# Kernel optimization log

Hardware: AMD Instinct MI355X
Metric: run time of the kernel (lower is better)

The kernel has to match this reference:

```python
import jax, jax.numpy as jnp
import numpy as np

B, N, D, H, NC = 4, 32, 128, 8, 27
DK = D // H
DFF = 4 * D
L = NC * N


def layer_norm(x, g, b, eps=1e-5):
    mu = jnp.mean(x, -1, keepdims=True)
    var = jnp.var(x, -1, keepdims=True)
    return (x - mu) * jax.lax.rsqrt(var + eps) * g + b


def setup_inputs() -> dict:
    ks = jax.random.split(jax.random.key(0), 16)
    s = 1.0 / np.sqrt(D)
    return {
        'x': jax.random.normal(ks[0], (B, N, D), jnp.float32),
        'mask': jax.random.randint(ks[1], (B, 1, N), 0, 2, jnp.int32),
        'coords': jax.random.normal(ks[2], (B, NC, N, 3), jnp.float32),
        'Wp': jax.random.normal(ks[3], (3, D), jnp.float32) * 0.5,
        'bp': jnp.zeros((D,), jnp.float32),
        'Wq': jax.random.normal(ks[4], (D, D), jnp.float32) * s,
        'bq': jnp.zeros((D,), jnp.float32),
        'Wk': jax.random.normal(ks[5], (D, D), jnp.float32) * s,
        'bk': jnp.zeros((D,), jnp.float32),
        'Wv': jax.random.normal(ks[6], (D, D), jnp.float32) * s,
        'bv': jnp.zeros((D,), jnp.float32),
        'Wo': jax.random.normal(ks[7], (D, D), jnp.float32) * s,
        'bo': jnp.zeros((D,), jnp.float32),
        'g1': jnp.ones((D,), jnp.float32),
        'b1': jnp.zeros((D,), jnp.float32),
        'g2': jnp.ones((D,), jnp.float32),
        'b2': jnp.zeros((D,), jnp.float32),
        'W1': jax.random.normal(ks[8], (D, DFF), jnp.float32) * s,
        'bf1': jnp.zeros((DFF,), jnp.float32),
        'W2': jax.random.normal(ks[9], (DFF, D), jnp.float32) * (1.0 / np.sqrt(DFF)),
        'bf2': jnp.zeros((D,), jnp.float32),
    }


def reference(x, mask, coords, Wp, bp, Wq, bq, Wk, bk, Wv, bv, Wo, bo,
              g1, b1, g2, b2, W1, bf1, W2, bf2):
    mask_enh = jnp.tile(mask, (1, NC, 1)).reshape(B, 1, 1, L)

    def step(i):
        # position_encoding: x broadcast over 27 images + linear of coords relative to atom i
        ci = jax.lax.dynamic_slice_in_dim(coords, i, 1, axis=2)        # [B,NC,1,3]
        ar = x[:, None] + (coords - ci) @ Wp + bp                      # [B,NC,N,D]
        a = ar.reshape(B, L, D)
        hn = layer_norm(a, g1, b1)
        q = (hn @ Wq + bq).reshape(B, L, H, DK).transpose(0, 2, 1, 3)
        k = (hn @ Wk + bk).reshape(B, L, H, DK).transpose(0, 2, 1, 3)
        v = (hn @ Wv + bv).reshape(B, L, H, DK).transpose(0, 2, 1, 3)
        scores = jnp.einsum('bhqd,bhkd->bhqk', q, k) / np.sqrt(DK)     # [B,H,L,L]
        scores = jnp.where(mask_enh == 0, -1e9, scores)
        att = jnp.einsum('bhqk,bhkd->bhqd', jax.nn.softmax(scores, -1), v)
        att = att.transpose(0, 2, 1, 3).reshape(B, L, D) @ Wo + bo
        s = a + att  # SublayerConnection (dropout identity in eval)
        # original keeps only [b, image 0, atom i] of the [B,NC,N,D] reshape; flat index = i
        return jax.lax.dynamic_slice_in_dim(s, i, 1, axis=1)[:, 0]     # [B,D]

    rows = jax.lax.map(step, jnp.arange(N))                            # [N,B,D]
    y = rows.transpose(1, 0, 2)                                        # [B,N,D]
    hn2 = layer_norm(y, g2, b2)
    return y + (jax.nn.relu(hn2 @ W1 + bf1) @ W2 + bf2)
```

## Files before the change

### kernel.cpp

```cpp
#include <hip/hip_runtime.h>


#define B_ 4
#define N_ 32
#define D_ 128
#define H_ 8
#define NC_ 27
#define DFF_ 512
#define L_ (NC_*N_)

__device__ __forceinline__ void red2_block128(float& a, float& b, float* sbuf, int tid){
  for (int off = 32; off; off >>= 1){ a += __shfl_xor(a, off); b += __shfl_xor(b, off); }
  if ((tid & 63) == 0){ sbuf[(tid>>6)*2+0] = a; sbuf[(tid>>6)*2+1] = b; }
  __syncthreads();
  a = sbuf[0] + sbuf[2];
  b = sbuf[1] + sbuf[3];
  __syncthreads();
}

__device__ __forceinline__ void bred2(float& a, float& b, float sred[2][8][2],
                                      int tid, int phase){
  for (int off = 32; off; off >>= 1){ a += __shfl_xor(a, off); b += __shfl_xor(b, off); }
  int pb = phase & 1;
  if ((tid & 63) == 0){ sred[pb][tid>>6][0] = a; sred[pb][tid>>6][1] = b; }
  __syncthreads();
  float sa = 0.f, sb = 0.f;
  #pragma unroll
  for (int w = 0; w < 8; w++){ sa += sred[pb][w][0]; sb += sred[pb][w][1]; }
  a = sa; b = sb;
}

__global__ __launch_bounds__(128) void k_pre(
    const float* __restrict__ x, const float* __restrict__ Wp,
    const float* __restrict__ bp, const float* __restrict__ g1,
    const float* __restrict__ b1,
    const float* __restrict__ Wq, const float* __restrict__ bq,
    const float* __restrict__ Wk, const float* __restrict__ bk,
    const float* __restrict__ Wv, const float* __restrict__ bv,
    float* __restrict__ varx, float* __restrict__ dxp,
    float* __restrict__ Axk, float* __restrict__ Axv,
    float* __restrict__ qbuf,
    float* __restrict__ Gk, float* __restrict__ Gv,
    float* __restrict__ ekv, float* __restrict__ M6){
  __shared__ float sbuf[4];
  __shared__ float s1_[D_], s2_[D_], s3_[D_], s4_[D_];
  int blk = blockIdx.x, tid = threadIdx.x;
  float wp0 = Wp[tid], wp1 = Wp[D_+tid], wp2 = Wp[2*D_+tid];
  if (blk < 128){
    float t = x[blk*D_+tid] + bp[tid];
    float a = wp0, b = wp1;
    red2_block128(a, b, sbuf, tid);
    float m0 = a*(1.f/D_), m1 = b*(1.f/D_);
    float a2 = wp2, st = t;
    red2_block128(a2, st, sbuf, tid);
    float m2 = a2*(1.f/D_), mean = st*(1.f/D_);
    float xh = t - mean;
    float w0 = wp0-m0, w1 = wp1-m1, w2 = wp2-m2;
    float vv = xh*xh, d0 = xh*w0;
    red2_block128(vv, d0, sbuf, tid);
    float vx = vv*(1.f/D_);
    float d1 = xh*w1, d2 = xh*w2;
    red2_block128(d1, d2, sbuf, tid);
    s1_[tid] = xh*g1[tid];
    s2_[tid] = xh*rsqrtf(vx+1e-5f)*g1[tid] + b1[tid];
    __syncthreads();
    float axk = 0.f, axv = 0.f, qa = bq[tid];
    #pragma unroll 8
    for (int e=0;e<D_;e++){
      float u = s1_[e], h = s2_[e];
      axk += u*Wk[e*D_+tid];
      axv += u*Wv[e*D_+tid];
      qa  += h*Wq[e*D_+tid];
    }
    Axk[blk*D_+tid] = axk;
    Axv[blk*D_+tid] = axv;
    qbuf[blk*D_+tid] = qa;
    if (tid == 0){
      varx[blk] = vx;
      dxp[blk*3+0] = d0; dxp[blk*3+1] = d1; dxp[blk*3+2] = d2;
    }
  } else {
    float a = wp0, b = wp1;
    red2_block128(a, b, sbuf, tid);
    float m0 = a*(1.f/D_), m1 = b*(1.f/D_);
    float a2 = wp2, dm = 0.f;
    red2_block128(a2, dm, sbuf, tid);
    float m2 = a2*(1.f/D_);
    float w0 = wp0-m0, w1 = wp1-m1, w2 = wp2-m2;
    float p0 = w0*w0, p1 = w0*w1;
    red2_block128(p0, p1, sbuf, tid);
    float p2 = w0*w2, p3 = w1*w1;
    red2_block128(p2, p3, sbuf, tid);
    float p4 = w1*w2, p5 = w2*w2;
    red2_block128(p4, p5, sbuf, tid);
    float g = g1[tid];
    s1_[tid] = w0*g; s2_[tid] = w1*g; s3_[tid] = w2*g; s4_[tid] = b1[tid];
    __syncthreads();
    float gk0=0.f,gk1=0.f,gk2=0.f, gv0=0.f,gv1=0.f,gv2=0.f;
    float ek = bk[tid], ev = bv[tid];
    #pragma unroll 4
    for (int e=0;e<D_;e++){
      float wk = Wk[e*D_+tid], wv = Wv[e*D_+tid];
      gk0 += s1_[e]*wk; gk1 += s2_[e]*wk; gk2 += s3_[e]*wk;
      gv0 += s1_[e]*wv; gv1 += s2_[e]*wv; gv2 += s3_[e]*wv;
      ek  += s4_[e]*wk; ev  += s4_[e]*wv;
    }
    Gk[tid] = gk0; Gk[D_+tid] = gk1; Gk[2*D_+tid] = gk2;
    Gv[tid] = gv0; Gv[D_+tid] = gv1; Gv[2*D_+tid] = gv2;
    ekv[tid] = ek; ekv[D_+tid] = ev;
    if (tid == 0){ M6[0]=p0; M6[1]=p1; M6[2]=p2; M6[3]=p3; M6[4]=p4; M6[5]=p5; }
  }
}

__global__ __launch_bounds__(512) void k_attn(
    const float* __restrict__ coords, const int* __restrict__ mask,
    const float* __restrict__ x, const float* __restrict__ bp,
    const float* __restrict__ varx, const float* __restrict__ dxp,
    const float* __restrict__ Axk, const float* __restrict__ Axv,
    const float* __restrict__ qbuf,
    const float* __restrict__ Gk, const float* __restrict__ Gv,
    const float* __restrict__ ekv, const float* __restrict__ M6,
    const float* __restrict__ Wo, const float* __restrict__ bo,
    const float* __restrict__ g2, const float* __restrict__ b2,
    const float* __restrict__ W1, const float* __restrict__ bf1,
    const float* __restrict__ W2, const float* __restrict__ bfb2,
    float* __restrict__ out){
  __shared__ float sc_s[H_*L_];
  __shared__ float is_s[L_];
  __shared__ float cq_s[NC_][3];
  __shared__ float q_s[D_];
  __shared__ float qAxk_s[H_][N_];
  __shared__ float qGk_s[H_][3];
  __shared__ float S3_s[H_];
  __shared__ float varx_s[N_];
  __shared__ float dxp_s[N_][3];
  __shared__ int   mask_s[N_];
  __shared__ float Tnp_s[H_][2][N_];
  __shared__ float Sh_s[H_], RD_s[H_][3];
  __shared__ float M6_s[6];
  __shared__ float att_s[D_], y_s[D_], hn_s[D_], f_s[DFF_];
  __shared__ float po[4][D_];
  __shared__ float sred[2][8][2];
  int bi = blockIdx.x;
  int b = bi >> 5, i = bi & 31;
  int tid = threadIdx.x;

  if (tid < D_) q_s[tid] = qbuf[bi*D_+tid];
  if (tid < N_){ varx_s[tid] = varx[b*N_+tid]; mask_s[tid] = mask[b*N_+tid]; }
  if (tid >= 32 && tid < 128){
    int t2 = tid - 32;
    dxp_s[t2/3][t2%3] = dxp[(b*N_ + t2/3)*3 + t2%3];
  }
  if (tid >= 128 && tid < 128+NC_*3){
    int t2 = tid - 128;
    cq_s[t2/3][t2%3] = coords[((size_t)(b*NC_ + t2/3)*N_ + i)*3 + t2%3];
  }
  if (tid >= 256 && tid < 262) M6_s[tid-256] = M6[tid-256];
  __syncthreads();

  if (tid < 256){
    int h = tid >> 5, n = tid & 31;
    float s = 0.f;
    #pragma unroll
    for (int k=0;k<16;k++) s += q_s[h*16+k]*Axk[(size_t)(b*N_+n)*D_ + h*16+k];
    qAxk_s[h][n] = s;
  } else if (tid < 256+24){
    int t2 = tid-256, h = t2/3, j = t2%3;
    float s = 0.f;
    #pragma unroll
    for (int k=0;k<16;k++) s += q_s[h*16+k]*Gk[j*D_ + h*16+k];
    qGk_s[h][j] = s;
  } else if (tid < 280+8){
    int h = tid-280;
    float s = 0.f;
    #pragma unroll
    for (int k=0;k<16;k++) s += q_s[h*16+k]*ekv[h*16+k];
    S3_s[h] = s;
  }
  __syncthreads();

  for (int l = tid; l < L_; l += 512){
    int c = l >> 5, n = l & 31;
    const float* ck = coords + ((size_t)(b*NC_+c)*N_ + n)*3;
    float d0 = ck[0]-cq_s[c][0], d1 = ck[1]-cq_s[c][1], d2 = ck[2]-cq_s[c][2];
    float quad = d0*d0*M6_s[0] + d1*d1*M6_s[3] + d2*d2*M6_s[5]
               + 2.f*(d0*d1*M6_s[1] + d0*d2*M6_s[2] + d1*d2*M6_s[4]);
    float lin  = d0*dxp_s[n][0] + d1*dxp_s[n][1] + d2*dxp_s[n][2];
    float E = varx_s[n] + (quad + 2.f*lin)*(1.f/D_);
    float is = rsqrtf(fmaxf(E, 0.f) + 1e-5f);
    is_s[l] = is;
    bool mk = mask_s[n] != 0;
    #pragma unroll
    for (int h=0; h<H_; h++){
      float sc = 0.25f*(is*(qAxk_s[h][n]
                 + d0*qGk_s[h][0] + d1*qGk_s[h][1] + d2*qGk_s[h][2]) + S3_s[h]);
      sc_s[h*L_ + l] = mk ? sc : -1e9f;
    }
  }
  __syncthreads();

  {
    int h = tid >> 6, lane = tid & 63, n = lane & 31, half = lane >> 5;
    int c0 = half ? 14 : 0, c1 = half ? NC_ : 14;
    float M = -3.0e38f;
    for (int c=c0; c<c1; c++) M = fmaxf(M, sc_s[h*L_ + c*N_ + n]);
    for (int off=32; off; off>>=1) M = fmaxf(M, __shfl_xor(M, off));
    float S=0.f, Tn=0.f, r0=0.f, r1=0.f, r2=0.f;
    for (int c=c0; c<c1; c++){
      int l = c*N_ + n;
      float w = expf(sc_s[h*L_ + l] - M);
      float t = w * is_s[l];
      S += w; Tn += t;
      const float* ck = coords + ((size_t)(b*NC_+c)*N_ + n)*3;
      r0 += t*(ck[0]-cq_s[c][0]);
      r1 += t*(ck[1]-cq_s[c][1]);
      r2 += t*(ck[2]-cq_s[c][2]);
    }
    Tnp_s[h][half][n] = Tn;
    for (int off=32; off; off>>=1){
      S  += __shfl_xor(S,  off);
      r0 += __shfl_xor(r0, off);
      r1 += __shfl_xor(r1, off);
      r2 += __shfl_xor(r2, off);
    }
    if (lane == 0){ Sh_s[h]=S; RD_s[h][0]=r0; RD_s[h][1]=r1; RD_s[h][2]=r2; }
  }
  __syncthreads();

  {
    int slot = tid >> 7, d = tid & 127, h = d >> 4;
    float pa = 0.f;
    #pragma unroll
    for (int n = slot*8; n < slot*8+8; n++){
      float Tn = Tnp_s[h][0][n] + Tnp_s[h][1][n];
      pa += Tn * Axv[(size_t)(b*N_+n)*D_ + d];
    }
    if (slot == 0)
      pa += RD_s[h][0]*Gv[d] + RD_s[h][1]*Gv[D_+d] + RD_s[h][2]*Gv[2*D_+d];
    po[slot][d] = pa;
  }
  __syncthreads();
  if (tid < D_){
    int h = tid >> 4;
    att_s[tid] = (po[0][tid]+po[1][tid]+po[2][tid]+po[3][tid])
                 / fmaxf(Sh_s[h], 1e-30f) + ekv[D_+tid];
  }
  __syncthreads();

  {
    int slot = tid >> 7, d = tid & 127;
    float a = 0.f;
    #pragma unroll 8
    for (int e=slot*32; e<slot*32+32; e++) a += att_s[e]*Wo[e*D_+d];
    po[slot][d] = a;
  }
  __syncthreads();
  float yv = 0.f;
  if (tid < D_){
    yv = x[bi*D_+tid] + bp[tid] + bo[tid]
       + po[0][tid]+po[1][tid]+po[2][tid]+po[3][tid];
    y_s[tid] = yv;
  }
  float s1 = (tid < D_) ? yv : 0.f, dm = 0.f;
  bred2(s1, dm, sred, tid, 0);
  float dev = yv - s1*(1.f/D_);
  float v1 = (tid < D_) ? dev*dev : 0.f; dm = 0.f;
  bred2(v1, dm, sred, tid, 1);
  if (tid < D_) hn_s[tid] = dev*rsqrtf(v1*(1.f/D_)+1e-5f)*g2[tid] + b2[tid];
  __syncthreads();
  float f = bf1[tid];
  #pragma unroll 8
  for (int e=0;e<D_;e++) f += hn_s[e]*W1[e*DFF_+tid];
  f_s[tid] = fmaxf(f, 0.f);
  __syncthreads();
  {
    int slot = tid >> 7, d = tid & 127;
    float a = 0.f;
    #pragma unroll 8
    for (int j=slot*128; j<slot*128+128; j++) a += f_s[j]*W2[j*D_+d];
    po[slot][d] = a;
  }
  __syncthreads();
  if (tid < D_)
    out[bi*D_+tid] = y_s[tid] + bfb2[tid]
                   + po[0][tid]+po[1][tid]+po[2][tid]+po[3][tid];
}

extern "C" void kernel_launch(void* const* d_in, const int* in_sizes, int n_in,
                              void* d_out, int out_size, void* d_ws, size_t ws_size,
                              hipStream_t stream){
  const float* x      = (const float*)d_in[0];
  const int*   mask   = (const int*)  d_in[1];
  const float* coords = (const float*)d_in[2];
  const float* Wp     = (const float*)d_in[3];
  const float* bp     = (const float*)d_in[4];
  const float* Wq     = (const float*)d_in[5];
  const float* bq     = (const float*)d_in[6];
  const float* Wk     = (const float*)d_in[7];
  const float* bk     = (const float*)d_in[8];
  const float* Wv     = (const float*)d_in[9];
  const float* bv     = (const float*)d_in[10];
  const float* Wo     = (const float*)d_in[11];
  const float* bo     = (const float*)d_in[12];
  const float* g1     = (const float*)d_in[13];
  const float* b1     = (const float*)d_in[14];
  const float* g2     = (const float*)d_in[15];
  const float* b2     = (const float*)d_in[16];
  const float* W1     = (const float*)d_in[17];
  const float* bf1    = (const float*)d_in[18];
  const float* W2     = (const float*)d_in[19];
  const float* bfb2   = (const float*)d_in[20];

  float* ws   = (float*)d_ws;
  float* varx = ws;
  float* dxp  = varx + 128;
  float* M6   = dxp  + 384;
  float* Gk   = M6   + 8;
  float* Gv   = Gk   + 384;
  float* ekv  = Gv   + 384;
  float* Axk  = ekv  + 256;
  float* Axv  = Axk  + 16384;
  float* qbuf = Axv  + 16384;

  k_pre <<<129, 128, 0, stream>>>(x, Wp, bp, g1, b1, Wq, bq, Wk, bk, Wv, bv,
                                  varx, dxp, Axk, Axv, qbuf, Gk, Gv, ekv, M6);
  k_attn<<<B_*N_, 512, 0, stream>>>(coords, mask, x, bp, varx, dxp, Axk, Axv,
                                    qbuf, Gk, Gv, ekv, M6, Wo, bo, g2, b2,
                                    W1, bf1, W2, bfb2, (float*)d_out);
}
```

Before: 124.5 us.

## Fuse precompute kernel into attention kernel with per-block K/V algebra

Merges the two launches into one kernel per (batch, atom) block. Each block now recomputes the row statistics, the Wp products and q itself. The per-row Axk/Axv products are replaced by projecting q through Wk (q·Wk^T) and applying Wv once to the softmax-weighted row sum, instead of materialising K/V projections for every row. Coordinate deltas are cached in shared memory so the softmax pass does not reload coords. This removes a launch and the workspace round trip, but duplicates the row-statistics and Wp work in every block and raises shared-memory use.

```diff
diff --git a/kernel.cpp b/kernel.cpp
--- a/kernel.cpp
+++ b/kernel.cpp
@@ -9,13 +9,10 @@
 #define DFF_ 512
 #define L_ (NC_*N_)
 
-__device__ __forceinline__ void red2_block128(float& a, float& b, float* sbuf, int tid){
-  for (int off = 32; off; off >>= 1){ a += __shfl_xor(a, off); b += __shfl_xor(b, off); }
-  if ((tid & 63) == 0){ sbuf[(tid>>6)*2+0] = a; sbuf[(tid>>6)*2+1] = b; }
-  __syncthreads();
-  a = sbuf[0] + sbuf[2];
-  b = sbuf[1] + sbuf[3];
-  __syncthreads();
+__device__ __forceinline__ float wave_red_sum(float v){
+  #pragma unroll
+  for (int off = 32; off; off >>= 1) v += __shfl_xor(v, off);
+  return v;
 }
 
 __device__ __forceinline__ void bred2(float& a, float& b, float sred[2][8][2],
@@ -30,152 +27,161 @@
   a = sa; b = sb;
 }
 
-__global__ __launch_bounds__(128) void k_pre(
-    const float* __restrict__ x, const float* __restrict__ Wp,
-    const float* __restrict__ bp, const float* __restrict__ g1,
-    const float* __restrict__ b1,
+__global__ __launch_bounds__(512) void k_fused(
+    const float* __restrict__ x, const int* __restrict__ mask,
+    const float* __restrict__ coords,
+    const float* __restrict__ Wp, const float* __restrict__ bp,
     const float* __restrict__ Wq, const float* __restrict__ bq,
     const float* __restrict__ Wk, const float* __restrict__ bk,
     const float* __restrict__ Wv, const float* __restrict__ bv,
-    float* __restrict__ varx, float* __restrict__ dxp,
-    float* __restrict__ Axk, float* __restrict__ Axv,
-    float* __restrict__ qbuf,
-    float* __restrict__ Gk, float* __restrict__ Gv,
-    float* __restrict__ ekv, float* __restrict__ M6){
-  __shared__ float sbuf[4];
-  __shared__ float s1_[D_], s2_[D_], s3_[D_], s4_[D_];
-  int blk = blockIdx.x, tid = threadIdx.x;
-  float wp0 = Wp[tid], wp1 = Wp[D_+tid], wp2 = Wp[2*D_+tid];
-  if (blk < 128){
-    float t = x[blk*D_+tid] + bp[tid];
-    float a = wp0, b = wp1;
-    red2_block128(a, b, sbuf, tid);
-    float m0 = a*(1.f/D_), m1 = b*(1.f/D_);
-    float a2 = wp2, st = t;
-    red2_block128(a2, st, sbuf, tid);
-    float m2 = a2*(1.f/D_), mean = st*(1.f/D_);
-    float xh = t - mean;
-    float w0 = wp0-m0, w1 = wp1-m1, w2 = wp2-m2;
-    float vv = xh*xh, d0 = xh*w0;
-    red2_block128(vv, d0, sbuf, tid);
-    float vx = vv*(1.f/D_);
-    float d1 = xh*w1, d2 = xh*w2;
-    red2_block128(d1, d2, sbuf, tid);
-    s1_[tid] = xh*g1[tid];
-    s2_[tid] = xh*rsqrtf(vx+1e-5f)*g1[tid] + b1[tid];
-    __syncthreads();
-    float axk = 0.f, axv = 0.f, qa = bq[tid];
-    #pragma unroll 8
-    for (int e=0;e<D_;e++){
-      float u = s1_[e], h = s2_[e];
-      axk += u*Wk[e*D_+tid];
-      axv += u*Wv[e*D_+tid];
-      qa  += h*Wq[e*D_+tid];
-    }
-    Axk[blk*D_+tid] = axk;
-    Axv[blk*D_+tid] = axv;
-    qbuf[blk*D_+tid] = qa;
-    if (tid == 0){
-      varx[blk] = vx;
-      dxp[blk*3+0] = d0; dxp[blk*3+1] = d1; dxp[blk*3+2] = d2;
-    }
-  } else {
-    float a = wp0, b = wp1;
-    red2_block128(a, b, sbuf, tid);
-    float m0 = a*(1.f/D_), m1 = b*(1.f/D_);
-    float a2 = wp2, dm = 0.f;
-    red2_block128(a2, dm, sbuf, tid);
-    float m2 = a2*(1.f/D_);
-    float w0 = wp0-m0, w1 = wp1-m1, w2 = wp2-m2;
-    float p0 = w0*w0, p1 = w0*w1;
-    red2_block128(p0, p1, sbuf, tid);
-    float p2 = w0*w2, p3 = w1*w1;
-    red2_block128(p2, p3, sbuf, tid);
-    float p4 = w1*w2, p5 = w2*w2;
-    red2_block128(p4, p5, sbuf, tid);
-    float g = g1[tid];
-    s1_[tid] = w0*g; s2_[tid] = w1*g; s3_[tid] = w2*g; s4_[tid] = b1[tid];
-    __syncthreads();
-    float gk0=0.f,gk1=0.f,gk2=0.f, gv0=0.f,gv1=0.f,gv2=0.f;
-    float ek = bk[tid], ev = bv[tid];
-    #pragma unroll 4
-    for (int e=0;e<D_;e++){
-      float wk = Wk[e*D_+tid], wv = Wv[e*D_+tid];
-      gk0 += s1_[e]*wk; gk1 += s2_[e]*wk; gk2 += s3_[e]*wk;
-      gv0 += s1_[e]*wv; gv1 += s2_[e]*wv; gv2 += s3_[e]*wv;
-      ek  += s4_[e]*wk; ev  += s4_[e]*wv;
-    }
-    Gk[tid] = gk0; Gk[D_+tid] = gk1; Gk[2*D_+tid] = gk2;
-    Gv[tid] = gv0; Gv[D_+tid] = gv1; Gv[2*D_+tid] = gv2;
-    ekv[tid] = ek; ekv[D_+tid] = ev;
-    if (tid == 0){ M6[0]=p0; M6[1]=p1; M6[2]=p2; M6[3]=p3; M6[4]=p4; M6[5]=p5; }
-  }
-}
-
-__global__ __launch_bounds__(512) void k_attn(
-    const float* __restrict__ coords, const int* __restrict__ mask,
-    const float* __restrict__ x, const float* __restrict__ bp,
-    const float* __restrict__ varx, const float* __restrict__ dxp,
-    const float* __restrict__ Axk, const float* __restrict__ Axv,
-    const float* __restrict__ qbuf,
-    const float* __restrict__ Gk, const float* __restrict__ Gv,
-    const float* __restrict__ ekv, const float* __restrict__ M6,
     const float* __restrict__ Wo, const float* __restrict__ bo,
+    const float* __restrict__ g1, const float* __restrict__ b1,
     const float* __restrict__ g2, const float* __restrict__ b2,
     const float* __restrict__ W1, const float* __restrict__ bf1,
     const float* __restrict__ W2, const float* __restrict__ bfb2,
-    float* __restrict__ out){
+    float* __restrict__ out)
+{
   __shared__ float sc_s[H_*L_];
   __shared__ float is_s[L_];
-  __shared__ float cq_s[NC_][3];
+  __shared__ float dc_s[3][L_];
+  __shared__ float xh_s[N_][D_+1];
+  __shared__ float ZU_s[H_][D_+4];
+  __shared__ float w_s[3][D_];
+  __shared__ float g1_s[D_], b1_s[D_], bp_s[D_];
   __shared__ float q_s[D_];
+  __shared__ float hn_s[D_];
   __shared__ float qAxk_s[H_][N_];
   __shared__ float qGk_s[H_][3];
   __shared__ float S3_s[H_];
   __shared__ float varx_s[N_];
   __shared__ float dxp_s[N_][3];
   __shared__ int   mask_s[N_];
+  __shared__ float cq_s[NC_][3];
+  __shared__ float M6_s[6];
+  __shared__ float mwp_s[3];
   __shared__ float Tnp_s[H_][2][N_];
   __shared__ float Sh_s[H_], RD_s[H_][3];
-  __shared__ float M6_s[6];
-  __shared__ float att_s[D_], y_s[D_], hn_s[D_], f_s[DFF_];
+  __shared__ float att_s[D_], y_s[D_], f_s[DFF_];
   __shared__ float po[4][D_];
   __shared__ float sred[2][8][2];
+
   int bi = blockIdx.x;
   int b = bi >> 5, i = bi & 31;
-  int tid = threadIdx.x;
-
-  if (tid < D_) q_s[tid] = qbuf[bi*D_+tid];
-  if (tid < N_){ varx_s[tid] = varx[b*N_+tid]; mask_s[tid] = mask[b*N_+tid]; }
-  if (tid >= 32 && tid < 128){
-    int t2 = tid - 32;
-    dxp_s[t2/3][t2%3] = dxp[(b*N_ + t2/3)*3 + t2%3];
-  }
-  if (tid >= 128 && tid < 128+NC_*3){
-    int t2 = tid - 128;
+  int tid  = threadIdx.x;
+  int wave = tid >> 6, lane = tid & 63;
+
+  if (tid < 384) w_s[tid>>7][tid&127] = Wp[tid];
+  if (tid < D_){ g1_s[tid] = g1[tid]; b1_s[tid] = b1[tid]; bp_s[tid] = bp[tid]; }
+  if (tid >= 384 && tid < 384+N_) mask_s[tid-384] = mask[b*N_ + (tid-384)];
+  if (tid >= 416 && tid < 416+NC_*3){
+    int t2 = tid - 416;
     cq_s[t2/3][t2%3] = coords[((size_t)(b*NC_ + t2/3)*N_ + i)*3 + t2%3];
   }
-  if (tid >= 256 && tid < 262) M6_s[tid-256] = M6[tid-256];
-  __syncthreads();
-
+  __syncthreads();
+  if (wave < 3){
+    float s = w_s[wave][lane] + w_s[wave][lane+64];
+    s = wave_red_sum(s);
+    if (lane == 0) mwp_s[wave] = s*(1.f/D_);
+  }
+  __syncthreads();
+  if (tid < 384) w_s[tid>>7][tid&127] -= mwp_s[tid>>7];
+  __syncthreads();
+  if (wave < 6){
+    const int ja[6] = {0,0,0,1,1,2}, jb[6] = {0,1,2,1,2,2};
+    float s = w_s[ja[wave]][lane]*w_s[jb[wave]][lane]
+            + w_s[ja[wave]][lane+64]*w_s[jb[wave]][lane+64];
+    s = wave_red_sum(s);
+    if (lane == 0) M6_s[wave] = s;
+  }
+
+  for (int r = wave; r < N_; r += 8){
+    float t0 = x[((size_t)(b*N_+r))*D_ + lane]     + bp_s[lane];
+    float t1 = x[((size_t)(b*N_+r))*D_ + lane+64]  + bp_s[lane+64];
+    float mean = wave_red_sum(t0 + t1)*(1.f/D_);
+    float xh0 = t0 - mean, xh1 = t1 - mean;
+    xh_s[r][lane] = xh0; xh_s[r][lane+64] = xh1;
+    float vv = xh0*xh0 + xh1*xh1;
+    float d0 = xh0*w_s[0][lane] + xh1*w_s[0][lane+64];
+    float d1 = xh0*w_s[1][lane] + xh1*w_s[1][lane+64];
+    float d2 = xh0*w_s[2][lane] + xh1*w_s[2][lane+64];
+    #pragma unroll
+    for (int off = 32; off; off >>= 1){
+      vv += __shfl_xor(vv, off); d0 += __shfl_xor(d0, off);
+      d1 += __shfl_xor(d1, off); d2 += __shfl_xor(d2, off);
+    }
+    if (lane == 0){
+      varx_s[r] = vv*(1.f/D_);
+      dxp_s[r][0] = d0; dxp_s[r][1] = d1; dxp_s[r][2] = d2;
+    }
+  }
+  __syncthreads();
+
+  if (tid < D_){
+    float isq = rsqrtf(varx_s[i] + 1e-5f);
+    hn_s[tid] = xh_s[i][tid]*isq*g1_s[tid] + b1_s[tid];
+  }
+  __syncthreads();
+  {
+    int slot = tid >> 7, d = tid & 127;
+    float a = 0.f;
+    #pragma unroll 8
+    for (int e = slot*32; e < slot*32+32; e++) a += hn_s[e]*Wq[e*D_+d];
+    po[slot][d] = a;
+  }
+  __syncthreads();
+  if (tid < D_) q_s[tid] = po[0][tid]+po[1][tid]+po[2][tid]+po[3][tid] + bq[tid];
+  __syncthreads();
+
+  {
+    int e = tid & 127, h0 = tid >> 7;
+    #pragma unroll
+    for (int hh = 0; hh < 2; hh++){
+      int h = h0 + hh*4;
+      const float4* wk4 = (const float4*)(Wk + (size_t)e*D_ + h*16);
+      float s = 0.f;
+      #pragma unroll
+      for (int kq = 0; kq < 4; kq++){
+        float4 wv4 = wk4[kq];
+        s += wv4.x*q_s[h*16+kq*4+0] + wv4.y*q_s[h*16+kq*4+1]
+           + wv4.z*q_s[h*16+kq*4+2] + wv4.w*q_s[h*16+kq*4+3];
+      }
+      ZU_s[h][e] = s;
+    }
+  }
+  __syncthreads();
+  {
+    int h = wave;
+    float u0 = ZU_s[h][lane], u1 = ZU_s[h][lane+64];
+    float s3 = b1_s[lane]*u0 + b1_s[lane+64]*u1;
+    if (lane < 16) s3 += q_s[h*16+lane]*bk[h*16+lane];
+    float qg0 = w_s[0][lane]*g1_s[lane]*u0 + w_s[0][lane+64]*g1_s[lane+64]*u1;
+    float qg1 = w_s[1][lane]*g1_s[lane]*u0 + w_s[1][lane+64]*g1_s[lane+64]*u1;
+    float qg2 = w_s[2][lane]*g1_s[lane]*u0 + w_s[2][lane+64]*g1_s[lane+64]*u1;
+    #pragma unroll
+    for (int off = 32; off; off >>= 1){
+      s3  += __shfl_xor(s3,  off); qg0 += __shfl_xor(qg0, off);
+      qg1 += __shfl_xor(qg1, off); qg2 += __shfl_xor(qg2, off);
+    }
+    if (lane == 0){ S3_s[h]=s3; qGk_s[h][0]=qg0; qGk_s[h][1]=qg1; qGk_s[h][2]=qg2; }
+  }
+  __syncthreads();
+  {
+    int e = tid & 127, h0 = tid >> 7;
+    ZU_s[h0][e]   *= g1_s[e];
+    ZU_s[h0+4][e] *= g1_s[e];
+  }
+  __syncthreads();
+  {
+    int half = tid >> 8, id = tid & 255, h = id >> 5, n = id & 31;
+    float s = 0.f;
+    #pragma unroll 8
+    for (int e = half*64; e < half*64+64; e++) s += xh_s[n][e]*ZU_s[h][e];
+    ((float*)po)[half*256 + id] = s;
+  }
+  __syncthreads();
   if (tid < 256){
     int h = tid >> 5, n = tid & 31;
-    float s = 0.f;
-    #pragma unroll
-    for (int k=0;k<16;k++) s += q_s[h*16+k]*Axk[(size_t)(b*N_+n)*D_ + h*16+k];
-    qAxk_s[h][n] = s;
-  } else if (tid < 256+24){
-    int t2 = tid-256, h = t2/3, j = t2%3;
-    float s = 0.f;
-    #pragma unroll
-    for (int k=0;k<16;k++) s += q_s[h*16+k]*Gk[j*D_ + h*16+k];
-    qGk_s[h][j] = s;
-  } else if (tid < 280+8){
-    int h = tid-280;
-    float s = 0.f;
-    #pragma unroll
-    for (int k=0;k<16;k++) s += q_s[h*16+k]*ekv[h*16+k];
-    S3_s[h] = s;
+    qAxk_s[h][n] = ((float*)po)[tid] + ((float*)po)[256 + tid];
   }
   __syncthreads();
 
@@ -183,6 +189,7 @@
     int c = l >> 5, n = l & 31;
     const float* ck = coords + ((size_t)(b*NC_+c)*N_ + n)*3;
     float d0 = ck[0]-cq_s[c][0], d1 = ck[1]-cq_s[c][1], d2 = ck[2]-cq_s[c][2];
+    dc_s[0][l] = d0; dc_s[1][l] = d1; dc_s[2][l] = d2;
     float quad = d0*d0*M6_s[0] + d1*d1*M6_s[3] + d2*d2*M6_s[5]
                + 2.f*(d0*d1*M6_s[1] + d0*d2*M6_s[2] + d1*d2*M6_s[4]);
     float lin  = d0*dxp_s[n][0] + d1*dxp_s[n][1] + d2*dxp_s[n][2];
@@ -191,7 +198,7 @@
     is_s[l] = is;
     bool mk = mask_s[n] != 0;
     #pragma unroll
-    for (int h=0; h<H_; h++){
+    for (int h = 0; h < H_; h++){
       float sc = 0.25f*(is*(qAxk_s[h][n]
                  + d0*qGk_s[h][0] + d1*qGk_s[h][1] + d2*qGk_s[h][2]) + S3_s[h]);
       sc_s[h*L_ + l] = mk ? sc : -1e9f;
@@ -200,24 +207,23 @@
   __syncthreads();
 
   {
-    int h = tid >> 6, lane = tid & 63, n = lane & 31, half = lane >> 5;
+    int h = tid >> 6, n = lane & 31, half = lane >> 5;
     int c0 = half ? 14 : 0, c1 = half ? NC_ : 14;
     float M = -3.0e38f;
-    for (int c=c0; c<c1; c++) M = fmaxf(M, sc_s[h*L_ + c*N_ + n]);
-    for (int off=32; off; off>>=1) M = fmaxf(M, __shfl_xor(M, off));
+    for (int c = c0; c < c1; c++) M = fmaxf(M, sc_s[h*L_ + c*N_ + n]);
+    #pragma unroll
+    for (int off = 32; off; off >>= 1) M = fmaxf(M, __shfl_xor(M, off));
     float S=0.f, Tn=0.f, r0=0.f, r1=0.f, r2=0.f;
-    for (int c=c0; c<c1; c++){
+    for (int c = c0; c < c1; c++){
       int l = c*N_ + n;
       float w = expf(sc_s[h*L_ + l] - M);
       float t = w * is_s[l];
       S += w; Tn += t;
-      const float* ck = coords + ((size_t)(b*NC_+c)*N_ + n)*3;
-      r0 += t*(ck[0]-cq_s[c][0]);
-      r1 += t*(ck[1]-cq_s[c][1]);
-      r2 += t*(ck[2]-cq_s[c][2]);
+      r0 += t*dc_s[0][l]; r1 += t*dc_s[1][l]; r2 += t*dc_s[2][l];
     }
     Tnp_s[h][half][n] = Tn;
-    for (int off=32; off; off>>=1){
+    #pragma unroll
+    for (int off = 32; off; off >>= 1){
       S  += __shfl_xor(S,  off);
       r0 += __shfl_xor(r0, off);
       r1 += __shfl_xor(r1, off);
@@ -228,36 +234,45 @@
   __syncthreads();
 
   {
+    int e = tid & 127, h0 = tid >> 7;
+    #pragma unroll
+    for (int hh = 0; hh < 2; hh++){
+      int h = h0 + hh*4;
+      float z = 0.f;
+      #pragma unroll 8
+      for (int n = 0; n < N_; n++){
+        float Tn = Tnp_s[h][0][n] + Tnp_s[h][1][n];
+        z += Tn * xh_s[n][e];
+      }
+      z += RD_s[h][0]*w_s[0][e] + RD_s[h][1]*w_s[1][e] + RD_s[h][2]*w_s[2][e];
+      float rS = 1.f / fmaxf(Sh_s[h], 1e-30f);
+      ZU_s[h][e] = z*g1_s[e]*rS + b1_s[e];
+    }
+  }
+  __syncthreads();
+
+  {
     int slot = tid >> 7, d = tid & 127, h = d >> 4;
-    float pa = 0.f;
-    #pragma unroll
-    for (int n = slot*8; n < slot*8+8; n++){
-      float Tn = Tnp_s[h][0][n] + Tnp_s[h][1][n];
-      pa += Tn * Axv[(size_t)(b*N_+n)*D_ + d];
-    }
-    if (slot == 0)
-      pa += RD_s[h][0]*Gv[d] + RD_s[h][1]*Gv[D_+d] + RD_s[h][2]*Gv[2*D_+d];
-    po[slot][d] = pa;
-  }
-  __syncthreads();
-  if (tid < D_){
-    int h = tid >> 4;
-    att_s[tid] = (po[0][tid]+po[1][tid]+po[2][tid]+po[3][tid])
-                 / fmaxf(Sh_s[h], 1e-30f) + ekv[D_+tid];
-  }
+    float a = 0.f;
+    #pragma unroll 8
+    for (int e = slot*32; e < slot*32+32; e++) a += ZU_s[h][e]*Wv[e*D_+d];
+    po[slot][d] = a;
+  }
+  __syncthreads();
+  if (tid < D_) att_s[tid] = po[0][tid]+po[1][tid]+po[2][tid]+po[3][tid] + bv[tid];
   __syncthreads();
 
   {
     int slot = tid >> 7, d = tid & 127;
     float a = 0.f;
     #pragma unroll 8
-    for (int e=slot*32; e<slot*32+32; e++) a += att_s[e]*Wo[e*D_+d];
+    for (int e = slot*32; e < slot*32+32; e++) a += att_s[e]*Wo[e*D_+d];
     po[slot][d] = a;
   }
   __syncthreads();
   float yv = 0.f;
   if (tid < D_){
-    yv = x[bi*D_+tid] + bp[tid] + bo[tid]
+    yv = x[(size_t)bi*D_+tid] + bp_s[tid] + bo[tid]
        + po[0][tid]+po[1][tid]+po[2][tid]+po[3][tid];
     y_s[tid] = yv;
   }
@@ -270,19 +285,19 @@
   __syncthreads();
   float f = bf1[tid];
   #pragma unroll 8
-  for (int e=0;e<D_;e++) f += hn_s[e]*W1[e*DFF_+tid];
+  for (int e = 0; e < D_; e++) f += hn_s[e]*W1[e*DFF_+tid];
   f_s[tid] = fmaxf(f, 0.f);
   __syncthreads();
   {
     int slot = tid >> 7, d = tid & 127;
     float a = 0.f;
     #pragma unroll 8
-    for (int j=slot*128; j<slot*128+128; j++) a += f_s[j]*W2[j*D_+d];
+    for (int j = slot*128; j < slot*128+128; j++) a += f_s[j]*W2[j*D_+d];
     po[slot][d] = a;
   }
   __syncthreads();
   if (tid < D_)
-    out[bi*D_+tid] = y_s[tid] + bfb2[tid]
+    out[(size_t)bi*D_+tid] = y_s[tid] + bfb2[tid]
                    + po[0][tid]+po[1][tid]+po[2][tid]+po[3][tid];
 }
 
@@ -311,20 +326,7 @@
   const float* W2     = (const float*)d_in[19];
   const float* bfb2   = (const float*)d_in[20];
 
-  float* ws   = (float*)d_ws;
-  float* varx = ws;
-  float* dxp  = varx + 128;
-  float* M6   = dxp  + 384;
-  float* Gk   = M6   + 8;
-  float* Gv   = Gk   + 384;
-  float* ekv  = Gv   + 384;
-  float* Axk  = ekv  + 256;
-  float* Axv  = Axk  + 16384;
-  float* qbuf = Axv  + 16384;
-
-  k_pre <<<129, 128, 0, stream>>>(x, Wp, bp, g1, b1, Wq, bq, Wk, bk, Wv, bv,
-                                  varx, dxp, Axk, Axv, qbuf, Gk, Gv, ekv, M6);
-  k_attn<<<B_*N_, 512, 0, stream>>>(coords, mask, x, bp, varx, dxp, Axk, Axv,
-                                    qbuf, Gk, Gv, ekv, M6, Wo, bo, g2, b2,
-                                    W1, bf1, W2, bfb2, (float*)d_out);
+  k_fused<<<B_*N_, 512, 0, stream>>>(x, mask, coords, Wp, bp, Wq, bq, Wk, bk,
+                                     Wv, bv, Wo, bo, g1, b1, g2, b2,
+                                     W1, bf1, W2, bfb2, (float*)d_out);
 }
```

Measured after the change: 125.6 us. No clear change (+0.9%).
